# Performance work log

Hardware: AMD Instinct MI355X
Metric: run time of the kernel (lower is better)

The kernel has to match this reference:

```python
import jax, jax.numpy as jnp
import numpy as np

H = 64
VOCAB = 64
SLOTS = 4
N_PASSES = 3
EPS = 1e-5


def _ln(x, g, b):
    m = jnp.mean(x, axis=-1, keepdims=True)
    v = jnp.mean((x - m) ** 2, axis=-1, keepdims=True)
    return (x - m) * jax.lax.rsqrt(v + EPS) * g + b


def setup_inputs() -> dict:
    key = jax.random.key(0)
    ks = iter(jax.random.split(key, 32))
    B, L = 128, 4096
    f = lambda shape, scale=0.05: jax.random.normal(next(ks), shape, dtype=jnp.float32) * scale
    inp = {
        "seq": jax.random.randint(next(ks), (B, L), 0, VOCAB),
        # Encoder
        "embed": f((VOCAB, H), 1.0),
        "ff1_w": f((H, 2 * H)), "ff1_b": jnp.zeros((2 * H,), jnp.float32),
        "ff2_w": f((2 * H, H)), "ff2_b": jnp.zeros((H,), jnp.float32),
        "enc_g": jnp.ones((H,), jnp.float32), "enc_b": jnp.zeros((H,), jnp.float32),
        # ForwardGate
        "g1_w": f((H, H // 2)), "g1_b": jnp.zeros((H // 2,), jnp.float32),
        "g2_w": f((H // 2, 1)), "g2_b": jnp.zeros((1,), jnp.float32),
        # Re-encoding layers (stacked over passes)
        "rq_w": f((N_PASSES, H, H)), "rq_b": jnp.zeros((N_PASSES, H), jnp.float32),
        "rk_w": f((N_PASSES, H, H)), "rk_b": jnp.zeros((N_PASSES, H), jnp.float32),
        "rv_w": f((N_PASSES, H, H)), "rv_b": jnp.zeros((N_PASSES, H), jnp.float32),
        "rn_g": jnp.ones((N_PASSES, H), jnp.float32), "rn_b": jnp.zeros((N_PASSES, H), jnp.float32),
        # ReadHead
        "rd_q_w": f((H, H)), "rd_q_b": jnp.zeros((H,), jnp.float32),
        "out_w": f((H, VOCAB)), "out_b": jnp.zeros((VOCAB,), jnp.float32),
    }
    return inp


def reference(seq, embed, ff1_w, ff1_b, ff2_w, ff2_b, enc_g, enc_b,
              g1_w, g1_b, g2_w, g2_b,
              rq_w, rq_b, rk_w, rk_b, rv_w, rv_b, rn_g, rn_b,
              rd_q_w, rd_q_b, out_w, out_b):
    scale = 1.0 / np.sqrt(H)
    # Encoder: embed + FFN residual + LayerNorm
    h = embed[seq]                                            # (B,L,H)
    ff = jax.nn.relu(h @ ff1_w + ff1_b) @ ff2_w + ff2_b
    hidden = _ln(h + ff, enc_g, enc_b)                        # (B,L,H)
    # Gate scores -> top-k slot selection
    scores = jax.nn.sigmoid(jax.nn.relu(hidden @ g1_w + g1_b) @ g2_w + g2_b)[..., 0]  # (B,L)
    _, idx = jax.lax.top_k(scores, SLOTS)                     # (B,k)
    slots = jnp.take_along_axis(hidden, idx[:, :, None], axis=1)  # (B,k,H)
    # Iterative cross-attention re-encoding
    for p in range(N_PASSES):
        Sq = slots @ rq_w[p] + rq_b[p]                        # (B,k,H)
        Sk = hidden @ rk_w[p] + rk_b[p]                       # (B,L,H)
        Sv = hidden @ rv_w[p] + rv_b[p]
        attn = jax.nn.softmax(jnp.einsum("bkh,blh->bkl", Sq, Sk) * scale, axis=-1)
        slots = _ln(slots + jnp.einsum("bkl,blh->bkh", attn, Sv), rn_g[p], rn_b[p])
    # Read head: attend last-token query over slots
    q = hidden[:, -1, :] @ rd_q_w + rd_q_b                    # (B,H)
    attn = jax.nn.softmax(jnp.einsum("bkh,bh->bk", slots, q) * scale, axis=-1)
    read = jnp.einsum("bk,bkh->bh", attn, slots)
    return read @ out_w + out_b                               # (B,VOCAB)
```

## Files before the change

kernel.cpp:

```cpp
#include <hip/hip_runtime.h>
#include <math.h>

#define H 64
#define VOCAB 64
#define LSEQ 4096
#define NSLOTS 4
#define NP 3
#define EPS 1e-5f

typedef unsigned long long ull;

__device__ __forceinline__ float wsum(float x) {
    #pragma unroll
    for (int m = 1; m < 64; m <<= 1) x += __shfl_xor(x, m);
    return x;
}
__device__ __forceinline__ float wmax(float x) {
    #pragma unroll
    for (int m = 1; m < 64; m <<= 1) x = fmaxf(x, __shfl_xor(x, m));
    return x;
}


__global__ __launch_bounds__(64) void build_all(
    const float* __restrict__ embed,
    const float* __restrict__ ff1_w, const float* __restrict__ ff1_b,
    const float* __restrict__ ff2_w, const float* __restrict__ ff2_b,
    const float* __restrict__ enc_g, const float* __restrict__ enc_b,
    const float* __restrict__ g1_w,  const float* __restrict__ g1_b,
    const float* __restrict__ g2_w,  const float* __restrict__ g2_b,
    const float* __restrict__ rq_w,  const float* __restrict__ rq_b,
    const float* __restrict__ rk_w,  const float* __restrict__ rk_b,
    const float* __restrict__ rv_w,  const float* __restrict__ rv_b,
    const float* __restrict__ rd_q_w, const float* __restrict__ rd_q_b,
    const float* __restrict__ out_w,
    float* __restrict__ enc_t, float* __restrict__ score_t,
    float* __restrict__ c_t, float* __restrict__ q_t,
    float* __restrict__ MT, float* __restrict__ SvT, float* __restrict__ owT)
{
    const int seg  = blockIdx.x >> 6;
    const int v    = blockIdx.x & 63;
    const int lane = threadIdx.x;

    __shared__ float h_s[H];
    __shared__ float a1[2 * H];
    __shared__ float hid_s[H];
    __shared__ float sk_s[H];

    h_s[lane] = embed[v * H + lane];
    __syncthreads();

    float pA[4] = {0, 0, 0, 0}, pB[4] = {0, 0, 0, 0};
    #pragma unroll
    for (int c4 = 0; c4 < 4; c4++)
        #pragma unroll
        for (int d = 0; d < 16; d++) {
            int dd = c4 * 16 + d;
            float hv = h_s[dd];
            pA[c4] += hv * ff1_w[dd * 128 + lane];
            pB[c4] += hv * ff1_w[dd * 128 + lane + 64];
        }
    a1[lane]      = fmaxf(ff1_b[lane]      + ((pA[0] + pA[1]) + (pA[2] + pA[3])), 0.f);
    a1[lane + 64] = fmaxf(ff1_b[lane + 64] + ((pB[0] + pB[1]) + (pB[2] + pB[3])), 0.f);
    __syncthreads();

    float pO[4] = {0, 0, 0, 0};
    #pragma unroll
    for (int c4 = 0; c4 < 4; c4++)
        #pragma unroll
        for (int j = 0; j < 32; j++) {
            int jj = c4 * 32 + j;
            pO[c4] += a1[jj] * ff2_w[jj * H + lane];
        }
    float o = ff2_b[lane] + ((pO[0] + pO[1]) + (pO[2] + pO[3]));

    float x = h_s[lane] + o;
    float s1 = x, s2 = x * x;
    #pragma unroll
    for (int m = 1; m < 64; m <<= 1) { s1 += __shfl_xor(s1, m); s2 += __shfl_xor(s2, m); }
    float mu  = s1 * (1.f / 64.f);
    float var = s2 * (1.f / 64.f) - mu * mu;
    float hid = (x - mu) * rsqrtf(var + EPS) * enc_g[lane] + enc_b[lane];
    hid_s[lane] = hid;
    __syncthreads();

    if (seg == 0) {
        enc_t[v * H + lane] = hid;
        float p = 0.f;
        if (lane < 32) {
            float a[2] = {0, 0};
            #pragma unroll
            for (int c2 = 0; c2 < 2; c2++)
                #pragma unroll
                for (int d = 0; d < 32; d++) {
                    int dd = c2 * 32 + d;
                    a[c2] += hid_s[dd] * g1_w[dd * 32 + lane];
                }
            p = fmaxf(g1_b[lane] + a[0] + a[1], 0.f) * g2_w[lane];
        }
        p = wsum(p);
        if (lane == 0) score_t[v] = 1.f / (1.f + expf(-(p + g2_b[0])));
        float qa[4] = {0, 0, 0, 0};
        #pragma unroll
        for (int c4 = 0; c4 < 4; c4++)
            #pragma unroll
            for (int d = 0; d < 16; d++) {
                int dd = c4 * 16 + d;
                qa[c4] += hid_s[dd] * rd_q_w[dd * H + lane];
            }
        q_t[v * H + lane] = rd_q_b[lane] + ((qa[0] + qa[1]) + (qa[2] + qa[3]));
    }

    if (seg < 3) {
        const int p = seg;
        float ka[4] = {0, 0, 0, 0};
        #pragma unroll
        for (int c4 = 0; c4 < 4; c4++)
            #pragma unroll
            for (int d = 0; d < 16; d++) {
                int dd = c4 * 16 + d;
                ka[c4] += hid_s[dd] * rk_w[(p * H + dd) * H + lane];
            }
        float skv = rk_b[p * H + lane] + ((ka[0] + ka[1]) + (ka[2] + ka[3]));
        sk_s[lane] = skv;
        float cpart = wsum(rq_b[p * H + lane] * skv);
        if (lane == 0) c_t[p * 64 + v] = cpart;
        __syncthreads();
        const float4* rw4 = (const float4*)(rq_w + (size_t)(p * 64 + lane) * 64);
        const float4* sk4 = (const float4*)sk_s;
        float ma[4] = {0, 0, 0, 0};
        #pragma unroll
        for (int i = 0; i < 16; i++) {
            float4 w4 = rw4[i];
            float4 s4v = sk4[i];
            ma[0] += w4.x * s4v.x; ma[1] += w4.y * s4v.y;
            ma[2] += w4.z * s4v.z; ma[3] += w4.w * s4v.w;
        }
        MT[p * 4096 + v * 64 + lane] = ((ma[0] + ma[1]) + (ma[2] + ma[3]));
    } else {
        const int p = seg - 3;
        float va[4] = {0, 0, 0, 0};
        #pragma unroll
        for (int c4 = 0; c4 < 4; c4++)
            #pragma unroll
            for (int d = 0; d < 16; d++) {
                int dd = c4 * 16 + d;
                va[c4] += hid_s[dd] * rv_w[(p * H + dd) * H + lane];
            }
        float svv = rv_b[p * H + lane] + ((va[0] + va[1]) + (va[2] + va[3]));
        SvT[p * 4096 + lane * 64 + v] = svv;
        if (seg == 3) owT[v * 64 + lane] = out_w[lane * 64 + v];
    }
}

#define PASS(P, MC, MN, CCV, RGV, RBV, LOADNEXT)                               \
{                                                                              \
    float4 vcur[16];                                                           \
    { const float4* b4 = (const float4*)(SvT + (P) * 4096 + lane * 64);        \
      _Pragma("unroll") for (int i = 0; i < 16; i++) vcur[i] = b4[i]; }        \
    if (LOADNEXT) {                                                            \
      const float4* b4 = (const float4*)(MT + ((P) + 1) * 4096 + lane * 64);   \
      _Pragma("unroll") for (int i = 0; i < 16; i++) MN[i] = b4[i]; }          \
    sls[wid][lane] = s;                                                        \
    const float4* sp = (const float4*)sls[wid];                                \
    float a0 = 0, a1x = 0, a2 = 0, a3 = 0;                                     \
    _Pragma("unroll") for (int i = 0; i < 16; i++) {                           \
        float4 s4v = sp[i];                                                    \
        a0 += s4v.x * MC[i].x; a1x += s4v.y * MC[i].y;                         \
        a2 += s4v.z * MC[i].z; a3 += s4v.w * MC[i].w; }                        \
    float lg = (CCV + ((a0 + a1x) + (a2 + a3))) * 0.125f;                      \
    float w  = cntf * __expf(lg);                                              \
    wls[wid][lane] = w;                                                        \
    float denom = wsum(w);                                                     \
    const float4* wp = (const float4*)wls[wid];                                \
    float b0 = 0, b1 = 0, b2 = 0, b3 = 0;                                      \
    _Pragma("unroll") for (int i = 0; i < 16; i++) {                           \
        float4 w4 = wp[i];                                                     \
        b0 += w4.x * vcur[i].x; b1 += w4.y * vcur[i].y;                        \
        b2 += w4.z * vcur[i].z; b3 += w4.w * vcur[i].w; }                      \
    float y = s * denom + ((b0 + b1) + (b2 + b3));                             \
    float s1 = y, s2v = y * y;                                                 \
    _Pragma("unroll") for (int m = 1; m < 64; m <<= 1) {                       \
        s1 += __shfl_xor(s1, m); s2v += __shfl_xor(s2v, m); }                  \
    float muy  = s1 * (1.f / 64.f);                                            \
    float vary = s2v * (1.f / 64.f) - muy * muy;                               \
    s = (y - muy) * rsqrtf(vary + EPS * denom * denom) * RGV + RBV;            \
}

__global__ __launch_bounds__(256) void run_batches(
    const int*   __restrict__ seq,
    const float* __restrict__ score_t, const float* __restrict__ enc_t,
    const float* __restrict__ c_t, const float* __restrict__ q_t,
    const float* __restrict__ MT, const float* __restrict__ SvT,
    const float* __restrict__ owT,
    const float* __restrict__ rn_g, const float* __restrict__ rn_b,
    const float* __restrict__ out_b,
    float* __restrict__ out)
{
    __shared__ int   whist[4][64];
    __shared__ float sls[4][64], wls[4][64], slN[4][64];
    __shared__ float l4[4];
    __shared__ float rbuf[64];

    const int bid = blockIdx.x, tid = threadIdx.x;
    const int wid = tid >> 6, lane = tid & 63;

    const int4* s4 = (const int4*)(seq + (size_t)bid * LSEQ);
    int4 t0 = s4[tid];
    int4 t1 = s4[tid + 256];
    int4 t2 = s4[tid + 512];
    int4 t3 = s4[tid + 768];
    const int last = seq[(size_t)bid * LSEQ + LSEQ - 1];

    whist[wid][lane] = 0;

    float sc  = score_t[lane];
    float cc0 = c_t[lane],      cc1 = c_t[64 + lane],  cc2 = c_t[128 + lane];
    float rg0 = rn_g[lane],     rg1 = rn_g[64 + lane], rg2 = rn_g[128 + lane];
    float rb0 = rn_b[lane],     rb1 = rn_b[64 + lane], rb2 = rn_b[128 + lane];
    float ob  = out_b[lane];

    float mxs  = wmax(sc);
    ull   bm   = __ballot(sc == mxs);
    int   t_star = __ffsll(bm) - 1;
    int   nmax   = __popcll(bm);

    float s = enc_t[t_star * 64 + lane];
    float q = q_t[last * 64 + lane];

    float4 mA[16], mB[16], vA[16];
    {
        const float4* p4 = (const float4*)(MT + lane * 64);
        #pragma unroll
        for (int i = 0; i < 16; i++) mA[i] = p4[i];
        const float4* q4 = (const float4*)(SvT + lane * 64);
        #pragma unroll
        for (int i = 0; i < 16; i++) vA[i] = q4[i];
    }

    float lg0 = 0.f;
    if (wid == 0) {
        sls[0][lane] = s;
        const float4* sp = (const float4*)sls[0];
        float a0 = 0, a1x = 0, a2 = 0, a3 = 0;
        #pragma unroll
        for (int i = 0; i < 16; i++) {
            float4 s4v = sp[i];
            a0 += s4v.x * mA[i].x; a1x += s4v.y * mA[i].y;
            a2 += s4v.z * mA[i].z; a3 += s4v.w * mA[i].w;
        }
        lg0 = (cc0 + ((a0 + a1x) + (a2 + a3))) * 0.125f;
    }

    {
        int* hw = whist[wid];
        atomicAdd(&hw[t0.x], 1); atomicAdd(&hw[t0.y], 1);
        atomicAdd(&hw[t0.z], 1); atomicAdd(&hw[t0.w], 1);
        atomicAdd(&hw[t1.x], 1); atomicAdd(&hw[t1.y], 1);
        atomicAdd(&hw[t1.z], 1); atomicAdd(&hw[t1.w], 1);
        atomicAdd(&hw[t2.x], 1); atomicAdd(&hw[t2.y], 1);
        atomicAdd(&hw[t2.z], 1); atomicAdd(&hw[t2.w], 1);
        atomicAdd(&hw[t3.x], 1); atomicAdd(&hw[t3.y], 1);
        atomicAdd(&hw[t3.z], 1); atomicAdd(&hw[t3.w], 1);
    }
    __syncthreads();

    const int cnt = whist[0][lane] + whist[1][lane] + whist[2][lane] + whist[3][lane];
    const float cntf = (float)cnt;
    const int cnt_ts = __shfl(cnt, t_star);
    const bool spec = (nmax == 1) && (cnt_ts >= NSLOTS);

    if (spec) {
        if (wid != 0) return;

        {
            const float4* b4 = (const float4*)(MT + 4096 + lane * 64);
            #pragma unroll
            for (int i = 0; i < 16; i++) mB[i] = b4[i];
            float w = cntf * __expf(lg0);
            wls[0][lane] = w;
            float denom = wsum(w);
            const float4* wp = (const float4*)wls[0];
            float b0 = 0, b1 = 0, b2 = 0, b3 = 0;
            #pragma unroll
            for (int i = 0; i < 16; i++) {
                float4 w4 = wp[i];
                b0 += w4.x * vA[i].x; b1 += w4.y * vA[i].y;
                b2 += w4.z * vA[i].z; b3 += w4.w * vA[i].w;
            }
            float y = s * denom + ((b0 + b1) + (b2 + b3));
            float s1 = y, s2v = y * y;
            #pragma unroll
            for (int m = 1; m < 64; m <<= 1) { s1 += __shfl_xor(s1, m); s2v += __shfl_xor(s2v, m); }
            float muy  = s1 * (1.f / 64.f);
            float vary = s2v * (1.f / 64.f) - muy * muy;
            s = (y - muy) * rsqrtf(vary + EPS * denom * denom) * rg0 + rb0;
        }
        PASS(1, mB, mA, cc1, rg1, rb1, 1)
        PASS(2, mA, mB, cc2, rg2, rb2, 0)

        float4 ow[16];
        {
            const float4* b4 = (const float4*)(owT + lane * 64);
            #pragma unroll
            for (int i = 0; i < 16; i++) ow[i] = b4[i];
        }
        rbuf[lane] = s;
        __builtin_amdgcn_wave_barrier();
        const float4* rp = (const float4*)rbuf;
        float o0 = ob, o1 = 0.f, o2 = 0.f, o3 = 0.f;
        #pragma unroll
        for (int i = 0; i < 16; i++) {
            float4 rv = rp[i];
            o0 += rv.x * ow[i].x; o1 += rv.y * ow[i].y;
            o2 += rv.z * ow[i].z; o3 += rv.w * ow[i].w;
        }
        out[(size_t)bid * VOCAB + lane] = ((o0 + o1) + (o2 + o3));
        return;
    }

    int my_tok = 0;
    {
        float key = cnt > 0 ? sc : -1.f;
        int filled = 0;
        bool have = false;
        #pragma unroll 1
        for (int r = 0; r < NSLOTS && filled < NSLOTS; r++) {
            float m2 = wmax(key);
            ull win = __ballot(key == m2);
            int tk = __ffsll(win) - 1;
            int c  = __shfl(cnt, tk);
            if (!have && (unsigned)(wid - filled) < (unsigned)c) { my_tok = tk; have = true; }
            filled += c;
            if (lane == tk) key = -1.f;
        }
    }

    s = enc_t[my_tok * 64 + lane];

    PASS(0, mA, mB, cc0, rg0, rb0, 1)
    PASS(1, mB, mA, cc1, rg1, rb1, 1)
    PASS(2, mA, mB, cc2, rg2, rb2, 0)

    float lk = wsum(s * q) * 0.125f;
    if (lane == 0) l4[wid] = lk;
    slN[wid][lane] = s;

    float4 ow[16];
    if (wid == 0) {
        const float4* b4 = (const float4*)(owT + lane * 64);
        #pragma unroll
        for (int i = 0; i < 16; i++) ow[i] = b4[i];
    }
    __syncthreads();

    if (wid == 0) {
        float e0 = __expf(l4[0]), e1 = __expf(l4[1]);
        float e2 = __expf(l4[2]), e3 = __expf(l4[3]);
        float dn = e0 + e1 + e2 + e3;
        float r = (e0 * slN[0][lane] + e1 * slN[1][lane]
                 + e2 * slN[2][lane] + e3 * slN[3][lane]) / dn;
        rbuf[lane] = r;
        __builtin_amdgcn_wave_barrier();
        const float4* rp = (const float4*)rbuf;
        float o0 = ob, o1 = 0.f, o2 = 0.f, o3 = 0.f;
        #pragma unroll
        for (int i = 0; i < 16; i++) {
            float4 rv = rp[i];
            o0 += rv.x * ow[i].x; o1 += rv.y * ow[i].y;
            o2 += rv.z * ow[i].z; o3 += rv.w * ow[i].w;
        }
        out[(size_t)bid * VOCAB + lane] = ((o0 + o1) + (o2 + o3));
    }
}

extern "C" void kernel_launch(void* const* d_in, const int* in_sizes, int n_in,
                              void* d_out, int out_size, void* d_ws, size_t ws_size,
                              hipStream_t stream) {
    const int*   seq    = (const int*)  d_in[0];
    const float* embed  = (const float*)d_in[1];
    const float* ff1_w  = (const float*)d_in[2];
    const float* ff1_b  = (const float*)d_in[3];
    const float* ff2_w  = (const float*)d_in[4];
    const float* ff2_b  = (const float*)d_in[5];
    const float* enc_g  = (const float*)d_in[6];
    const float* enc_b  = (const float*)d_in[7];
    const float* g1_w   = (const float*)d_in[8];
    const float* g1_b   = (const float*)d_in[9];
    const float* g2_w   = (const float*)d_in[10];
    const float* g2_b   = (const float*)d_in[11];
    const float* rq_w   = (const float*)d_in[12];
    const float* rq_b   = (const float*)d_in[13];
    const float* rk_w   = (const float*)d_in[14];
    const float* rk_b   = (const float*)d_in[15];
    const float* rv_w   = (const float*)d_in[16];
    const float* rv_b   = (const float*)d_in[17];
    const float* rn_g   = (const float*)d_in[18];
    const float* rn_b   = (const float*)d_in[19];
    const float* rd_q_w = (const float*)d_in[20];
    const float* rd_q_b = (const float*)d_in[21];
    const float* out_w  = (const float*)d_in[22];
    const float* out_b  = (const float*)d_in[23];
    float* out = (float*)d_out;

    const int B = in_sizes[0] / LSEQ;

    float* ws      = (float*)d_ws;
    float* enc_t   = ws;
    float* score_t = ws + 4096;
    float* c_t     = ws + 4160;
    float* q_t     = ws + 4352;
    float* MT      = ws + 8448;
    float* SvT     = ws + 20736;
    float* owT     = ws + 33024;

    build_all<<<384, 64, 0, stream>>>(
        embed, ff1_w, ff1_b, ff2_w, ff2_b, enc_g, enc_b,
        g1_w, g1_b, g2_w, g2_b,
        rq_w, rq_b, rk_w, rk_b, rv_w, rv_b,
        rd_q_w, rd_q_b, out_w,
        enc_t, score_t, c_t, q_t, MT, SvT, owT);

    run_batches<<<B, 256, 0, stream>>>(
        seq, score_t, enc_t, c_t, q_t, MT, SvT, owT,
        rn_g, rn_b, out_b, out);
}
```

Before: 22.76 us.

## Move token histogram into the build kernel and pack build work four waves per block

Result: slower. 24.75 us (+8.7%).

```diff
diff --git a/kernel.cpp b/kernel.cpp
--- a/kernel.cpp
+++ b/kernel.cpp
@@ -7,6 +7,7 @@
 #define NSLOTS 4
 #define NP 3
 #define EPS 1e-5f
+#define NBUILD 96
 
 typedef unsigned long long ull;
 
@@ -22,7 +23,8 @@
 }
 
 
-__global__ __launch_bounds__(64) void build_all(
+__global__ __launch_bounds__(256) void build_and_hist(
+    const int*   __restrict__ seq,
     const float* __restrict__ embed,
     const float* __restrict__ ff1_w, const float* __restrict__ ff1_b,
     const float* __restrict__ ff2_w, const float* __restrict__ ff2_b,
@@ -36,121 +38,153 @@
     const float* __restrict__ out_w,
     float* __restrict__ enc_t, float* __restrict__ score_t,
     float* __restrict__ c_t, float* __restrict__ q_t,
-    float* __restrict__ MT, float* __restrict__ SvT, float* __restrict__ owT)
+    float* __restrict__ MT, float* __restrict__ SvT, float* __restrict__ owT,
+    float* __restrict__ cnts_ws, int* __restrict__ lasts_ws)
 {
-    const int seg  = blockIdx.x >> 6;
-    const int v    = blockIdx.x & 63;
-    const int lane = threadIdx.x;
-
-    __shared__ float h_s[H];
-    __shared__ float a1[2 * H];
-    __shared__ float hid_s[H];
-    __shared__ float sk_s[H];
-
-    h_s[lane] = embed[v * H + lane];
-    __syncthreads();
-
-    float pA[4] = {0, 0, 0, 0}, pB[4] = {0, 0, 0, 0};
-    #pragma unroll
-    for (int c4 = 0; c4 < 4; c4++)
-        #pragma unroll
-        for (int d = 0; d < 16; d++) {
-            int dd = c4 * 16 + d;
-            float hv = h_s[dd];
-            pA[c4] += hv * ff1_w[dd * 128 + lane];
-            pB[c4] += hv * ff1_w[dd * 128 + lane + 64];
-        }
-    a1[lane]      = fmaxf(ff1_b[lane]      + ((pA[0] + pA[1]) + (pA[2] + pA[3])), 0.f);
-    a1[lane + 64] = fmaxf(ff1_b[lane + 64] + ((pB[0] + pB[1]) + (pB[2] + pB[3])), 0.f);
-    __syncthreads();
-
-    float pO[4] = {0, 0, 0, 0};
-    #pragma unroll
-    for (int c4 = 0; c4 < 4; c4++)
-        #pragma unroll
-        for (int j = 0; j < 32; j++) {
-            int jj = c4 * 32 + j;
-            pO[c4] += a1[jj] * ff2_w[jj * H + lane];
-        }
-    float o = ff2_b[lane] + ((pO[0] + pO[1]) + (pO[2] + pO[3]));
-
-    float x = h_s[lane] + o;
-    float s1 = x, s2 = x * x;
-    #pragma unroll
-    for (int m = 1; m < 64; m <<= 1) { s1 += __shfl_xor(s1, m); s2 += __shfl_xor(s2, m); }
-    float mu  = s1 * (1.f / 64.f);
-    float var = s2 * (1.f / 64.f) - mu * mu;
-    float hid = (x - mu) * rsqrtf(var + EPS) * enc_g[lane] + enc_b[lane];
-    hid_s[lane] = hid;
-    __syncthreads();
-
-    if (seg == 0) {
-        enc_t[v * H + lane] = hid;
-        float p = 0.f;
-        if (lane < 32) {
-            float a[2] = {0, 0};
-            #pragma unroll
-            for (int c2 = 0; c2 < 2; c2++)
-                #pragma unroll
-                for (int d = 0; d < 32; d++) {
-                    int dd = c2 * 32 + d;
-                    a[c2] += hid_s[dd] * g1_w[dd * 32 + lane];
-                }
-            p = fmaxf(g1_b[lane] + a[0] + a[1], 0.f) * g2_w[lane];
-        }
-        p = wsum(p);
-        if (lane == 0) score_t[v] = 1.f / (1.f + expf(-(p + g2_b[0])));
-        float qa[4] = {0, 0, 0, 0};
+    __shared__ float bld[4][320];
+    __shared__ int   whist[4][64];
+
+    const int bid = blockIdx.x, tid = threadIdx.x;
+    const int wid = tid >> 6, lane = tid & 63;
+
+    if (bid < NBUILD) {
+        const int t   = bid * 4 + wid;
+        const int seg = t >> 6, v = t & 63;
+        float* h_s   = bld[wid];
+        float* a1p   = bld[wid] + 64;
+        float* hid_s = bld[wid] + 192;
+        float* sk_s  = bld[wid] + 256;
+
+        h_s[lane] = embed[v * H + lane];
+        __builtin_amdgcn_wave_barrier();
+
+        float pA[4] = {0, 0, 0, 0}, pB[4] = {0, 0, 0, 0};
         #pragma unroll
         for (int c4 = 0; c4 < 4; c4++)
             #pragma unroll
             for (int d = 0; d < 16; d++) {
                 int dd = c4 * 16 + d;
-                qa[c4] += hid_s[dd] * rd_q_w[dd * H + lane];
-            }
-        q_t[v * H + lane] = rd_q_b[lane] + ((qa[0] + qa[1]) + (qa[2] + qa[3]));
-    }
-
-    if (seg < 3) {
-        const int p = seg;
-        float ka[4] = {0, 0, 0, 0};
+                float hv = h_s[dd];
+                pA[c4] += hv * ff1_w[dd * 128 + lane];
+                pB[c4] += hv * ff1_w[dd * 128 + lane + 64];
+            }
+        a1p[lane]      = fmaxf(ff1_b[lane]      + ((pA[0] + pA[1]) + (pA[2] + pA[3])), 0.f);
+        a1p[lane + 64] = fmaxf(ff1_b[lane + 64] + ((pB[0] + pB[1]) + (pB[2] + pB[3])), 0.f);
+        __builtin_amdgcn_wave_barrier();
+
+        float pO[4] = {0, 0, 0, 0};
         #pragma unroll
         for (int c4 = 0; c4 < 4; c4++)
             #pragma unroll
-            for (int d = 0; d < 16; d++) {
-                int dd = c4 * 16 + d;
-                ka[c4] += hid_s[dd] * rk_w[(p * H + dd) * H + lane];
-            }
-        float skv = rk_b[p * H + lane] + ((ka[0] + ka[1]) + (ka[2] + ka[3]));
-        sk_s[lane] = skv;
-        float cpart = wsum(rq_b[p * H + lane] * skv);
-        if (lane == 0) c_t[p * 64 + v] = cpart;
-        __syncthreads();
-        const float4* rw4 = (const float4*)(rq_w + (size_t)(p * 64 + lane) * 64);
-        const float4* sk4 = (const float4*)sk_s;
-        float ma[4] = {0, 0, 0, 0};
-        #pragma unroll
-        for (int i = 0; i < 16; i++) {
-            float4 w4 = rw4[i];
-            float4 s4v = sk4[i];
-            ma[0] += w4.x * s4v.x; ma[1] += w4.y * s4v.y;
-            ma[2] += w4.z * s4v.z; ma[3] += w4.w * s4v.w;
-        }
-        MT[p * 4096 + v * 64 + lane] = ((ma[0] + ma[1]) + (ma[2] + ma[3]));
-    } else {
-        const int p = seg - 3;
-        float va[4] = {0, 0, 0, 0};
-        #pragma unroll
-        for (int c4 = 0; c4 < 4; c4++)
-            #pragma unroll
-            for (int d = 0; d < 16; d++) {
-                int dd = c4 * 16 + d;
-                va[c4] += hid_s[dd] * rv_w[(p * H + dd) * H + lane];
-            }
-        float svv = rv_b[p * H + lane] + ((va[0] + va[1]) + (va[2] + va[3]));
-        SvT[p * 4096 + lane * 64 + v] = svv;
-        if (seg == 3) owT[v * 64 + lane] = out_w[lane * 64 + v];
-    }
+            for (int j = 0; j < 32; j++) {
+                int jj = c4 * 32 + j;
+                pO[c4] += a1p[jj] * ff2_w[jj * H + lane];
+            }
+        float o = ff2_b[lane] + ((pO[0] + pO[1]) + (pO[2] + pO[3]));
+
+        float x = h_s[lane] + o;
+        float s1 = x, s2 = x * x;
+        #pragma unroll
+        for (int m = 1; m < 64; m <<= 1) { s1 += __shfl_xor(s1, m); s2 += __shfl_xor(s2, m); }
+        float mu  = s1 * (1.f / 64.f);
+        float var = s2 * (1.f / 64.f) - mu * mu;
+        float hid = (x - mu) * rsqrtf(var + EPS) * enc_g[lane] + enc_b[lane];
+        hid_s[lane] = hid;
+        __builtin_amdgcn_wave_barrier();
+
+        if (seg == 0) {
+            enc_t[v * H + lane] = hid;
+            float p = 0.f;
+            if (lane < 32) {
+                float a[2] = {0, 0};
+                #pragma unroll
+                for (int c2 = 0; c2 < 2; c2++)
+                    #pragma unroll
+                    for (int d = 0; d < 32; d++) {
+                        int dd = c2 * 32 + d;
+                        a[c2] += hid_s[dd] * g1_w[dd * 32 + lane];
+                    }
+                p = fmaxf(g1_b[lane] + a[0] + a[1], 0.f) * g2_w[lane];
+            }
+            p = wsum(p);
+            if (lane == 0) score_t[v] = 1.f / (1.f + expf(-(p + g2_b[0])));
+            float qa[4] = {0, 0, 0, 0};
+            #pragma unroll
+            for (int c4 = 0; c4 < 4; c4++)
+                #pragma unroll
+                for (int d = 0; d < 16; d++) {
+                    int dd = c4 * 16 + d;
+                    qa[c4] += hid_s[dd] * rd_q_w[dd * H + lane];
+                }
+            q_t[v * H + lane] = rd_q_b[lane] + ((qa[0] + qa[1]) + (qa[2] + qa[3]));
+        }
+        if (seg < 3) {
+            const int p = seg;
+            float ka[4] = {0, 0, 0, 0};
+            #pragma unroll
+            for (int c4 = 0; c4 < 4; c4++)
+                #pragma unroll
+                for (int d = 0; d < 16; d++) {
+                    int dd = c4 * 16 + d;
+                    ka[c4] += hid_s[dd] * rk_w[(p * H + dd) * H + lane];
+                }
+            float skv = rk_b[p * H + lane] + ((ka[0] + ka[1]) + (ka[2] + ka[3]));
+            sk_s[lane] = skv;
+            float cpart = wsum(rq_b[p * H + lane] * skv);
+            if (lane == 0) c_t[p * 64 + v] = cpart;
+            __builtin_amdgcn_wave_barrier();
+            const float4* rw4 = (const float4*)(rq_w + (size_t)(p * 64 + lane) * 64);
+            const float4* sk4 = (const float4*)sk_s;
+            float ma[4] = {0, 0, 0, 0};
+            #pragma unroll
+            for (int i = 0; i < 16; i++) {
+                float4 w4 = rw4[i];
+                float4 s4v = sk4[i];
+                ma[0] += w4.x * s4v.x; ma[1] += w4.y * s4v.y;
+                ma[2] += w4.z * s4v.z; ma[3] += w4.w * s4v.w;
+            }
+            MT[p * 4096 + v * 64 + lane] = ((ma[0] + ma[1]) + (ma[2] + ma[3]));
+        } else {
+            const int p = seg - 3;
+            float va[4] = {0, 0, 0, 0};
+            #pragma unroll
+            for (int c4 = 0; c4 < 4; c4++)
+                #pragma unroll
+                for (int d = 0; d < 16; d++) {
+                    int dd = c4 * 16 + d;
+                    va[c4] += hid_s[dd] * rv_w[(p * H + dd) * H + lane];
+                }
+            float svv = rv_b[p * H + lane] + ((va[0] + va[1]) + (va[2] + va[3]));
+            SvT[p * 4096 + lane * 64 + v] = svv;
+            if (seg == 3) owT[v * 64 + lane] = out_w[lane * 64 + v];
+        }
+        return;
+    }
+
+    const int b = bid - NBUILD;
+    const int4* s4 = (const int4*)(seq + (size_t)b * LSEQ);
+    int4 t0 = s4[tid];
+    int4 t1 = s4[tid + 256];
+    int4 t2 = s4[tid + 512];
+    int4 t3 = s4[tid + 768];
+    whist[wid][lane] = 0;
+    __builtin_amdgcn_wave_barrier();
+    {
+        int* hw = whist[wid];
+        atomicAdd(&hw[t0.x], 1); atomicAdd(&hw[t0.y], 1);
+        atomicAdd(&hw[t0.z], 1); atomicAdd(&hw[t0.w], 1);
+        atomicAdd(&hw[t1.x], 1); atomicAdd(&hw[t1.y], 1);
+        atomicAdd(&hw[t1.z], 1); atomicAdd(&hw[t1.w], 1);
+        atomicAdd(&hw[t2.x], 1); atomicAdd(&hw[t2.y], 1);
+        atomicAdd(&hw[t2.z], 1); atomicAdd(&hw[t2.w], 1);
+        atomicAdd(&hw[t3.x], 1); atomicAdd(&hw[t3.y], 1);
+        atomicAdd(&hw[t3.z], 1); atomicAdd(&hw[t3.w], 1);
+    }
+    __syncthreads();
+    if (tid < 64)
+        cnts_ws[b * 64 + tid] =
+            (float)(whist[0][tid] + whist[1][tid] + whist[2][tid] + whist[3][tid]);
+    if (tid == 255) lasts_ws[b] = t3.w;
 }
 
 #define PASS(P, MC, MN, CCV, RGV, RBV, LOADNEXT)                               \
@@ -188,16 +222,15 @@
 }
 
 __global__ __launch_bounds__(256) void run_batches(
-    const int*   __restrict__ seq,
     const float* __restrict__ score_t, const float* __restrict__ enc_t,
     const float* __restrict__ c_t, const float* __restrict__ q_t,
     const float* __restrict__ MT, const float* __restrict__ SvT,
     const float* __restrict__ owT,
     const float* __restrict__ rn_g, const float* __restrict__ rn_b,
     const float* __restrict__ out_b,
+    const float* __restrict__ cnts_ws, const int* __restrict__ lasts_ws,
     float* __restrict__ out)
 {
-    __shared__ int   whist[4][64];
     __shared__ float sls[4][64], wls[4][64], slN[4][64];
     __shared__ float l4[4];
     __shared__ float rbuf[64];
@@ -205,78 +238,50 @@
     const int bid = blockIdx.x, tid = threadIdx.x;
     const int wid = tid >> 6, lane = tid & 63;
 
-    const int4* s4 = (const int4*)(seq + (size_t)bid * LSEQ);
-    int4 t0 = s4[tid];
-    int4 t1 = s4[tid + 256];
-    int4 t2 = s4[tid + 512];
-    int4 t3 = s4[tid + 768];
-    const int last = seq[(size_t)bid * LSEQ + LSEQ - 1];
-
-    whist[wid][lane] = 0;
-
+    const float cntf = cnts_ws[bid * 64 + lane];
     float sc  = score_t[lane];
-    float cc0 = c_t[lane],      cc1 = c_t[64 + lane],  cc2 = c_t[128 + lane];
-    float rg0 = rn_g[lane],     rg1 = rn_g[64 + lane], rg2 = rn_g[128 + lane];
-    float rb0 = rn_b[lane],     rb1 = rn_b[64 + lane], rb2 = rn_b[128 + lane];
+    float cc0 = c_t[lane],  cc1 = c_t[64 + lane],  cc2 = c_t[128 + lane];
+    float rg0 = rn_g[lane], rg1 = rn_g[64 + lane], rg2 = rn_g[128 + lane];
+    float rb0 = rn_b[lane], rb1 = rn_b[64 + lane], rb2 = rn_b[128 + lane];
     float ob  = out_b[lane];
+
+    float4 mA[16], mB[16], vA[16];
+    {
+        const float4* p4 = (const float4*)(MT + lane * 64);
+        #pragma unroll
+        for (int i = 0; i < 16; i++) mA[i] = p4[i];
+        const float4* q4 = (const float4*)(SvT + lane * 64);
+        #pragma unroll
+        for (int i = 0; i < 16; i++) vA[i] = q4[i];
+    }
 
     float mxs  = wmax(sc);
     ull   bm   = __ballot(sc == mxs);
     int   t_star = __ffsll(bm) - 1;
     int   nmax   = __popcll(bm);
-
-    float s = enc_t[t_star * 64 + lane];
-    float q = q_t[last * 64 + lane];
-
-    float4 mA[16], mB[16], vA[16];
-    {
-        const float4* p4 = (const float4*)(MT + lane * 64);
-        #pragma unroll
-        for (int i = 0; i < 16; i++) mA[i] = p4[i];
-        const float4* q4 = (const float4*)(SvT + lane * 64);
-        #pragma unroll
-        for (int i = 0; i < 16; i++) vA[i] = q4[i];
-    }
-
-    float lg0 = 0.f;
-    if (wid == 0) {
-        sls[0][lane] = s;
-        const float4* sp = (const float4*)sls[0];
-        float a0 = 0, a1x = 0, a2 = 0, a3 = 0;
-        #pragma unroll
-        for (int i = 0; i < 16; i++) {
-            float4 s4v = sp[i];
-            a0 += s4v.x * mA[i].x; a1x += s4v.y * mA[i].y;
-            a2 += s4v.z * mA[i].z; a3 += s4v.w * mA[i].w;
-        }
-        lg0 = (cc0 + ((a0 + a1x) + (a2 + a3))) * 0.125f;
-    }
-
-    {
-        int* hw = whist[wid];
-        atomicAdd(&hw[t0.x], 1); atomicAdd(&hw[t0.y], 1);
-        atomicAdd(&hw[t0.z], 1); atomicAdd(&hw[t0.w], 1);
-        atomicAdd(&hw[t1.x], 1); atomicAdd(&hw[t1.y], 1);
-        atomicAdd(&hw[t1.z], 1); atomicAdd(&hw[t1.w], 1);
-        atomicAdd(&hw[t2.x], 1); atomicAdd(&hw[t2.y], 1);
-        atomicAdd(&hw[t2.z], 1); atomicAdd(&hw[t2.w], 1);
-        atomicAdd(&hw[t3.x], 1); atomicAdd(&hw[t3.y], 1);
-        atomicAdd(&hw[t3.z], 1); atomicAdd(&hw[t3.w], 1);
-    }
-    __syncthreads();
-
-    const int cnt = whist[0][lane] + whist[1][lane] + whist[2][lane] + whist[3][lane];
-    const float cntf = (float)cnt;
-    const int cnt_ts = __shfl(cnt, t_star);
-    const bool spec = (nmax == 1) && (cnt_ts >= NSLOTS);
+    float cnt_ts = __shfl(cntf, t_star);
+    const bool spec = (nmax == 1) && (cnt_ts >= 4.f);
 
     if (spec) {
         if (wid != 0) return;
+        float s = enc_t[t_star * 64 + lane];
 
         {
+            sls[0][lane] = s;
+            const float4* sp = (const float4*)sls[0];
+            float a0 = 0, a1x = 0, a2 = 0, a3 = 0;
+            #pragma unroll
+            for (int i = 0; i < 16; i++) {
+                float4 s4v = sp[i];
+                a0 += s4v.x * mA[i].x; a1x += s4v.y * mA[i].y;
+                a2 += s4v.z * mA[i].z; a3 += s4v.w * mA[i].w;
+            }
+            float lg0 = (cc0 + ((a0 + a1x) + (a2 + a3))) * 0.125f;
+
             const float4* b4 = (const float4*)(MT + 4096 + lane * 64);
             #pragma unroll
             for (int i = 0; i < 16; i++) mB[i] = b4[i];
+
             float w = cntf * __expf(lg0);
             wls[0][lane] = w;
             float denom = wsum(w);
@@ -318,6 +323,10 @@
         out[(size_t)bid * VOCAB + lane] = ((o0 + o1) + (o2 + o3));
         return;
     }
+
+    const int cnt = (int)cntf;
+    const int last = lasts_ws[bid];
+    float q = q_t[last * 64 + lane];
 
     int my_tok = 0;
     {
@@ -336,7 +345,7 @@
         }
     }
 
-    s = enc_t[my_tok * 64 + lane];
+    float s = enc_t[my_tok * 64 + lane];
 
     PASS(0, mA, mB, cc0, rg0, rb0, 1)
     PASS(1, mB, mA, cc1, rg1, rb1, 1)
@@ -413,15 +422,17 @@
     float* MT      = ws + 8448;
     float* SvT     = ws + 20736;
     float* owT     = ws + 33024;
-
-    build_all<<<384, 64, 0, stream>>>(
-        embed, ff1_w, ff1_b, ff2_w, ff2_b, enc_g, enc_b,
+    float* cnts_ws = ws + 37120;
+    int*   lasts_ws = (int*)(ws + 37120 + (size_t)B * 64);
+
+    build_and_hist<<<NBUILD + B, 256, 0, stream>>>(
+        seq, embed, ff1_w, ff1_b, ff2_w, ff2_b, enc_g, enc_b,
         g1_w, g1_b, g2_w, g2_b,
         rq_w, rq_b, rk_w, rk_b, rv_w, rv_b,
         rd_q_w, rd_q_b, out_w,
-        enc_t, score_t, c_t, q_t, MT, SvT, owT);
+        enc_t, score_t, c_t, q_t, MT, SvT, owT, cnts_ws, lasts_ws);
 
     run_batches<<<B, 256, 0, stream>>>(
-        seq, score_t, enc_t, c_t, q_t, MT, SvT, owT,
-        rn_g, rn_b, out_b, out);
-}
+        score_t, enc_t, c_t, q_t, MT, SvT, owT,
+        rn_g, rn_b, out_b, cnts_ws, lasts_ws, out);
+}
```
